# Performance work log

Hardware: AMD Instinct MI355X
Metric: run time of the kernel (lower is better)

Reference implementation:

```python
import jax, jax.numpy as jnp
import numpy as np
from jax import lax

WIN = 8
SHIFT = 4
NUM_HEADS = 8
DIM = 256
HIDDEN = 1024  # dim * mlp_ratio
EPS = 1e-5


def _layer_norm(x, g, b):
    mu = jnp.mean(x, axis=-1, keepdims=True)
    var = jnp.var(x, axis=-1, keepdims=True)
    return (x - mu) * lax.rsqrt(var + EPS) * g + b


def _window_partition(x, w):
    # x: [B,H,W,C] -> [B*nW, w*w, C]
    B, H, W, C = x.shape
    x = x.reshape(B, H // w, w, W // w, w, C)
    x = x.transpose(0, 1, 3, 2, 4, 5)
    return x.reshape(-1, w * w, C)


def _window_reverse(win, w, H, W):
    C = win.shape[-1]
    B = win.shape[0] // ((H // w) * (W // w))
    x = win.reshape(B, H // w, W // w, w, w, C)
    x = x.transpose(0, 1, 3, 2, 4, 5)
    return x.reshape(B, H, W, C)


def _rel_pos_index(w):
    coords = np.stack(np.meshgrid(np.arange(w), np.arange(w), indexing='ij'))
    cf = coords.reshape(2, -1)
    rel = cf[:, :, None] - cf[:, None, :]
    rel = rel.transpose(1, 2, 0).astype(np.int64)
    rel[:, :, 0] += w - 1
    rel[:, :, 1] += w - 1
    rel[:, :, 0] *= 2 * w - 1
    return rel.sum(-1)  # [w*w, w*w]


def _shift_mask(H, W, w, s):
    img = np.zeros((1, H, W, 1), dtype=np.float32)
    slices = (slice(0, -w), slice(-w, -s), slice(-s, None))
    cnt = 0
    for hs in slices:
        for ws in slices:
            img[:, hs, ws, :] = cnt
            cnt += 1
    mw = img.reshape(1, H // w, w, W // w, w, 1).transpose(0, 1, 3, 2, 4, 5).reshape(-1, w * w)
    diff = mw[:, None, :] - mw[:, :, None]
    return jnp.asarray(np.where(diff != 0, -100.0, 0.0).astype(np.float32))  # [nW,N,N]


def setup_inputs() -> dict:
    key = jax.random.key(0)
    ks = jax.random.split(key, 10)
    d, hid, h = DIM, HIDDEN, NUM_HEADS
    inp = {
        'x': jax.random.normal(ks[0], (2, 16384, d), dtype=jnp.float32),
        'norm1_g': jnp.ones((d,), jnp.float32),
        'norm1_b': jnp.zeros((d,), jnp.float32),
        'qkv_w': jax.random.normal(ks[1], (d, 3 * d), jnp.float32) * 0.02,
        'qkv_b': jnp.zeros((3 * d,), jnp.float32),
        'rel_bias_table': jax.random.normal(ks[2], ((2 * WIN - 1) ** 2, h), jnp.float32) * 0.02,
        'proj_w': jax.random.normal(ks[3], (d, d), jnp.float32) * 0.02,
        'proj_b': jnp.zeros((d,), jnp.float32),
        'norm2_g': jnp.ones((d,), jnp.float32),
        'norm2_b': jnp.zeros((d,), jnp.float32),
        'lin1_w': jax.random.normal(ks[4], (d, hid), jnp.float32) * 0.02,
        'lin1_b': jnp.zeros((hid,), jnp.float32),
        'dw_w': jax.random.normal(ks[5], (hid, 1, 3, 3), jnp.float32) * 0.1,
        'dw_b': jnp.zeros((hid,), jnp.float32),
        'lin2_w': jax.random.normal(ks[6], (hid, d), jnp.float32) * 0.02,
        'lin2_b': jnp.zeros((d,), jnp.float32),
    }
    return inp


def _forward(x, norm1_g, norm1_b, qkv_w, qkv_b, rel_bias_table, proj_w, proj_b,
             norm2_g, norm2_b, lin1_w, lin1_b, dw_w, dw_b, lin2_w, lin2_b):
    B, L, C = x.shape
    H = W = int(np.sqrt(L))
    h, dh = NUM_HEADS, C // NUM_HEADS
    N = WIN * WIN

    shortcut = x
    y = _layer_norm(x, norm1_g, norm1_b).reshape(B, H, W, C)
    if SHIFT > 0:
        y = jnp.roll(y, shift=(-SHIFT, -SHIFT), axis=(1, 2))
        attn_mask = _shift_mask(H, W, WIN, SHIFT)  # [nW,N,N]
    else:
        attn_mask = None

    xw = _window_partition(y, WIN)  # [B_, N, C]
    B_ = xw.shape[0]

    qkv = (xw @ qkv_w + qkv_b).reshape(B_, N, 3, h, dh).transpose(2, 0, 3, 1, 4)
    q, k, v = qkv[0], qkv[1], qkv[2]  # [B_, h, N, dh]
    q = q * (dh ** -0.5)
    attn = jnp.einsum('bhnd,bhmd->bhnm', q, k)

    rpi = _rel_pos_index(WIN)  # [N,N] numpy
    bias = rel_bias_table[rpi.reshape(-1)].reshape(N, N, h).transpose(2, 0, 1)
    attn = attn + bias[None]

    if attn_mask is not None:
        nW = attn_mask.shape[0]
        attn = attn.reshape(B_ // nW, nW, h, N, N) + attn_mask[None, :, None]
        attn = attn.reshape(B_, h, N, N)

    attn = jax.nn.softmax(attn, axis=-1)
    out = jnp.einsum('bhnm,bhmd->bhnd', attn, v).transpose(0, 2, 1, 3).reshape(B_, N, C)
    out = out @ proj_w + proj_b

    y = _window_reverse(out, WIN, H, W)
    if SHIFT > 0:
        y = jnp.roll(y, shift=(SHIFT, SHIFT), axis=(1, 2))
    x = shortcut + y.reshape(B, L, C)

    # LeFF
    z = _layer_norm(x, norm2_g, norm2_b)
    z = jax.nn.gelu(z @ lin1_w + lin1_b, approximate=False)
    z = z.reshape(B, H, W, HIDDEN).transpose(0, 3, 1, 2)  # NCHW
    z = lax.conv_general_dilated(z, dw_w, (1, 1), 'SAME',
                                 feature_group_count=HIDDEN,
                                 dimension_numbers=('NCHW', 'OIHW', 'NCHW'))
    z = jax.nn.gelu(z + dw_b[None, :, None, None], approximate=False)
    z = z.transpose(0, 2, 3, 1).reshape(B, L, HIDDEN)
    z = z @ lin2_w + lin2_b
    return x + z


def reference(x, norm1_g, norm1_b, qkv_w, qkv_b, rel_bias_table, proj_w, proj_b,
              norm2_g, norm2_b, lin1_w, lin1_b, dw_w, dw_b, lin2_w, lin2_b):
    return _forward(x, norm1_g, norm1_b, qkv_w, qkv_b, rel_bias_table, proj_w, proj_b,
                    norm2_g, norm2_b, lin1_w, lin1_b, dw_w, dw_b, lin2_w, lin2_b)
```

## Files before the change

### kernel.cpp

```cpp
#include <hip/hip_runtime.h>
#include <math.h>

#define BATCH 2
#define HW 128
#define CDIM 256
#define LTOK 16384
#define MTOK 32768
#define HEADS 8
#define DH 32
#define WINSZ 8
#define NWIN 64
#define HID 1024

typedef unsigned int  u32;
typedef unsigned short u16;

typedef __attribute__((ext_vector_type(8))) short bf16x8;
typedef __attribute__((ext_vector_type(4))) float f32x4;

__device__ __forceinline__ float gelu_f(float v) {
    return 0.5f * v * (1.f + erff(v * 0.70710678118654752f));
}

__device__ __forceinline__ u16 f2bf(float f) {
    u32 u = __float_as_uint(f);
    u32 r = (u + 0x7fffu + ((u >> 16) & 1u)) >> 16;
    return (u16)r;
}

__device__ __forceinline__ float4 ld4(const float* p) { return *(const float4*)p; }
__device__ __forceinline__ float4 ld4(const u16* p) {
    uint2 v = *(const uint2*)p;
    float4 r;
    r.x = __uint_as_float((v.x & 0xffffu) << 16);
    r.y = __uint_as_float(v.x & 0xffff0000u);
    r.z = __uint_as_float((v.y & 0xffffu) << 16);
    r.w = __uint_as_float(v.y & 0xffff0000u);
    return r;
}
__device__ __forceinline__ void st4(float* p, float4 v) { *(float4*)p = v; }
__device__ __forceinline__ void st4(u16* p, float4 v) {
    uint2 o;
    o.x = (u32)f2bf(v.x) | ((u32)f2bf(v.y) << 16);
    o.y = (u32)f2bf(v.z) | ((u32)f2bf(v.w) << 16);
    *(uint2*)p = o;
}
__device__ __forceinline__ float lds1(const float* p) { return *p; }
__device__ __forceinline__ float lds1(const u16* p) { return __uint_as_float(((u32)*p) << 16); }
__device__ __forceinline__ void sts1(float* p, float v) { *p = v; }
__device__ __forceinline__ void sts1(u16* p, float v) { *p = f2bf(v); }

__device__ __forceinline__ void ld8bf(const u16* p, float* v) {
    uint4 r = *(const uint4*)p;
    v[0] = __uint_as_float((r.x & 0xffffu) << 16);
    v[1] = __uint_as_float(r.x & 0xffff0000u);
    v[2] = __uint_as_float((r.y & 0xffffu) << 16);
    v[3] = __uint_as_float(r.y & 0xffff0000u);
    v[4] = __uint_as_float((r.z & 0xffffu) << 16);
    v[5] = __uint_as_float(r.z & 0xffff0000u);
    v[6] = __uint_as_float((r.w & 0xffffu) << 16);
    v[7] = __uint_as_float(r.w & 0xffff0000u);
}

__device__ __forceinline__ void glds16(const u16* g, u16* l) {
    __builtin_amdgcn_global_load_lds(
        (const __attribute__((address_space(1))) unsigned int*)g,
        (__attribute__((address_space(3))) unsigned int*)l, 16, 0, 0);
}

__global__ __launch_bounds__(256) void transpose_bf16_kernel(
    const float* __restrict__ in, u16* __restrict__ out, int K, int N)
{
    __shared__ float t[32][33];
    int bn = blockIdx.x * 32, bk = blockIdx.y * 32;
    int tx = threadIdx.x & 31, ty = threadIdx.x >> 5;
    #pragma unroll
    for (int i = 0; i < 32; i += 8)
        t[ty + i][tx] = in[(size_t)(bk + ty + i) * N + bn + tx];
    __syncthreads();
    #pragma unroll
    for (int i = 0; i < 32; i += 8)
        out[(size_t)(bn + ty + i) * K + bk + tx] = f2bf(t[tx][ty + i]);
}

__global__ __launch_bounds__(256) void dwprep_kernel(
    const float* __restrict__ in, float* __restrict__ out)
{
    int idx = blockIdx.x * 256 + threadIdx.x;
    if (idx < 9 * HID) {
        int ch = idx / 9, t = idx - ch * 9;
        out[t * HID + ch] = in[idx];
    }
}

template<typename TI, typename TO>
__global__ __launch_bounds__(256) void ln_kernel(
    const TI* __restrict__ x, const float* __restrict__ g,
    const float* __restrict__ b, TO* __restrict__ y)
{
    int wave = threadIdx.x >> 6;
    int lane = threadIdx.x & 63;
    int row = blockIdx.x * 4 + wave;
    const TI* xr = x + (size_t)row * CDIM;
    float4 v = ld4(&xr[lane * 4]);
    float s  = v.x + v.y + v.z + v.w;
    float s2 = v.x*v.x + v.y*v.y + v.z*v.z + v.w*v.w;
    #pragma unroll
    for (int off = 32; off > 0; off >>= 1) {
        s  += __shfl_xor(s,  off);
        s2 += __shfl_xor(s2, off);
    }
    float mu   = s * (1.f / CDIM);
    float var  = s2 * (1.f / CDIM) - mu * mu;
    float rstd = rsqrtf(var + 1e-5f);
    float4 gv = *(const float4*)&g[lane * 4];
    float4 bv = *(const float4*)&b[lane * 4];
    float4 o;
    o.x = (v.x - mu) * rstd * gv.x + bv.x;
    o.y = (v.y - mu) * rstd * gv.y + bv.y;
    o.z = (v.z - mu) * rstd * gv.z + bv.z;
    o.w = (v.w - mu) * rstd * gv.w + bv.w;
    st4(&y[(size_t)row * CDIM + lane * 4], o);
}

template<int EPI, int K, typename TR, typename TO>
__global__ __launch_bounds__(256) void mgemm_kernel(
    const u16* __restrict__ A, const u16* __restrict__ Bt,
    const float* __restrict__ bias, const TR* __restrict__ res,
    TO* __restrict__ Cc, int N, int gx)
{
    __shared__ u16 As[128 * 64];
    __shared__ u16 Bs[128 * 64];

    int tid  = threadIdx.x;
    int lane = tid & 63;
    int wave = tid >> 6;
    int l15  = lane & 15;
    int hi   = lane >> 4;
    int wr = wave >> 1, wc = wave & 1;

    int nwg = gridDim.x;
    int bid = blockIdx.x;
    int swz = (bid & 7) * (nwg >> 3) + (bid >> 3);
    int bx = swz % gx, by = swz / gx;
    size_t bm = (size_t)by * 128;
    size_t bn = (size_t)bx * 128;

    int srow8 = lane >> 3;
    int ce    = (lane & 7) * 8;

    int ar = wr * 64 + l15;
    int br = wc * 64 + l15;

    f32x4 acc[4][4] = {};

    for (int t = 0; t < K / 64; ++t) {
        int kt = t * 64;
        #pragma unroll
        for (int g = 0; g < 4; ++g) {
            int rowb = wave * 32 + g * 8;
            int row  = rowb + srow8;
            int col  = kt + (ce ^ ((row & 7) << 3));
            glds16(A  + (bm + row) * K + col, As + rowb * 64);
            glds16(Bt + (bn + row) * K + col, Bs + rowb * 64);
        }
        __syncthreads();

        #pragma unroll
        for (int ks = 0; ks < 2; ++ks) {
            int e = ks * 32 + hi * 8;
            bf16x8 af[4], bfv[4];
            #pragma unroll
            for (int m = 0; m < 4; ++m) {
                int row = ar + m * 16;
                af[m] = *(const bf16x8*)&As[row * 64 + (e ^ ((row & 7) << 3))];
            }
            #pragma unroll
            for (int n = 0; n < 4; ++n) {
                int row = br + n * 16;
                bfv[n] = *(const bf16x8*)&Bs[row * 64 + (e ^ ((row & 7) << 3))];
            }
            #pragma unroll
            for (int m = 0; m < 4; ++m)
                #pragma unroll
                for (int n = 0; n < 4; ++n)
                    acc[m][n] = __builtin_amdgcn_mfma_f32_16x16x32_bf16(
                        af[m], bfv[n], acc[m][n], 0, 0, 0);
        }
        __syncthreads();
    }

    int colb = (int)bn + wc * 64 + l15;
    int rowb = (int)bm + wr * 64 + hi * 4;
    #pragma unroll
    for (int n = 0; n < 4; ++n) {
        float bv = bias[colb + n * 16];
        #pragma unroll
        for (int m = 0; m < 4; ++m) {
            #pragma unroll
            for (int r = 0; r < 4; ++r) {
                int row = rowb + m * 16 + r;
                float v = acc[m][n][r] + bv;
                if (EPI == 1) v += lds1(&res[(size_t)row * N + colb + n * 16]);
                if (EPI == 2) v = gelu_f(v);
                sts1(&Cc[(size_t)row * N + colb + n * 16], v);
            }
        }
    }
}

__global__ __launch_bounds__(512) void fused_qkv_attn_kernel(
    const u16* __restrict__ yn, const u16* __restrict__ qkv_wt,
    const float* __restrict__ qkv_b, const float* __restrict__ bias_table,
    u16* __restrict__ out)
{
    __shared__ u16 lds[8][4096];

    int tid  = threadIdx.x;
    int lane = tid & 63;
    int head = tid >> 6;
    int l15  = lane & 15;
    int hi   = lane >> 4;
    int w  = blockIdx.x;
    int b  = w >> 8;
    int ww = w & 255;
    int wr = ww >> 4, wc = ww & 15;
    u16* L = lds[head];

    auto tokof = [&](int n) -> int {
        int si = (wr * WINSZ + (n >> 3) + 4) & 127;
        int sj = (wc * WINSZ + (n & 7) + 4) & 127;
        return b * LTOK + si * HW + sj;
    };
    auto labelof = [&](int n) -> int {
        int i = wr * WINSZ + (n >> 3);
        int j = wc * WINSZ + (n & 7);
        int li = (i < 120) ? 0 : (i < 124 ? 1 : 2);
        int lj = (j < 120) ? 0 : (j < 124 ? 1 : 2);
        return li * 3 + lj;
    };

    const u16* arow[4];
    #pragma unroll
    for (int m = 0; m < 4; ++m)
        arow[m] = yn + (size_t)tokof(m * 16 + l15) * CDIM + hi * 8;

    f32x4 qa[4][2] = {}, ka[4][2] = {};
    #pragma unroll
    for (int kb = 0; kb < 8; ++kb) {
        bf16x8 a[4];
        #pragma unroll
        for (int m = 0; m < 4; ++m)
            a[m] = *(const bf16x8*)(arow[m] + kb * 32);
        #pragma unroll
        for (int nf = 0; nf < 2; ++nf) {
            const u16* wp = qkv_wt +
                (size_t)(head * 32 + nf * 16 + l15) * CDIM + kb * 32 + hi * 8;
            bf16x8 bq = *(const bf16x8*)wp;
            bf16x8 bk = *(const bf16x8*)(wp + 256 * CDIM);
            #pragma unroll
            for (int m = 0; m < 4; ++m) {
                qa[m][nf] = __builtin_amdgcn_mfma_f32_16x16x32_bf16(a[m], bq, qa[m][nf], 0, 0, 0);
                ka[m][nf] = __builtin_amdgcn_mfma_f32_16x16x32_bf16(a[m], bk, ka[m][nf], 0, 0, 0);
            }
        }
    }
    #pragma unroll
    for (int nf = 0; nf < 2; ++nf) {
        int d = nf * 16 + l15;
        float bq = qkv_b[head * 32 + d];
        float bk = qkv_b[256 + head * 32 + d];
        int g = nf * 2 + (l15 >> 3);
        #pragma unroll
        for (int m = 0; m < 4; ++m)
            #pragma unroll
            for (int r = 0; r < 4; ++r) {
                int tok = m * 16 + hi * 4 + r;
                int ad = tok * 32 + ((g ^ r ^ hi) << 3) + (d & 7);
                L[ad]        = f2bf(qa[m][nf][r] + bq);
                L[2048 + ad] = f2bf(ka[m][nf][r] + bk);
            }
    }
    bf16x8 qf[4], kf[4];
    {
        int sz = (hi ^ (l15 & 3) ^ ((l15 >> 2) & 3)) << 3;
        #pragma unroll
        for (int m = 0; m < 4; ++m) {
            int ra = (m * 16 + l15) * 32 + sz;
            qf[m] = *(const bf16x8*)&L[ra];
            kf[m] = *(const bf16x8*)&L[2048 + ra];
        }
    }

    f32x4 va[4][2] = {};
    #pragma unroll
    for (int kb = 0; kb < 8; ++kb) {
        bf16x8 a[4];
        #pragma unroll
        for (int m = 0; m < 4; ++m)
            a[m] = *(const bf16x8*)(arow[m] + kb * 32);
        #pragma unroll
        for (int nf = 0; nf < 2; ++nf) {
            const u16* wp = qkv_wt +
                (size_t)(512 + head * 32 + nf * 16 + l15) * CDIM + kb * 32 + hi * 8;
            bf16x8 bv = *(const bf16x8*)wp;
            #pragma unroll
            for (int m = 0; m < 4; ++m)
                va[m][nf] = __builtin_amdgcn_mfma_f32_16x16x32_bf16(a[m], bv, va[m][nf], 0, 0, 0);
        }
    }
    #pragma unroll
    for (int nf = 0; nf < 2; ++nf) {
        int d = nf * 16 + l15;
        float bv = qkv_b[512 + head * 32 + d];
        #pragma unroll
        for (int m = 0; m < 4; ++m)
            #pragma unroll
            for (int r = 0; r < 4; ++r) {
                int tok = m * 16 + hi * 4 + r;
                int av = d * 64 + (((tok >> 3) ^ (d & 7)) << 3) + (tok & 7);
                L[av] = f2bf(va[m][nf][r] + bv);
            }
    }
    bf16x8 vf[2][2];
    #pragma unroll
    for (int nf = 0; nf < 2; ++nf) {
        int d = nf * 16 + l15;
        #pragma unroll
        for (int ks = 0; ks < 2; ++ks) {
            int rv = d * 64 + (((ks * 4 + hi) ^ (d & 7)) << 3);
            vf[nf][ks] = *(const bf16x8*)&L[rv];
        }
    }

    f32x4 s[4][4];
    #pragma unroll
    for (int m = 0; m < 4; ++m)
        #pragma unroll
        for (int n = 0; n < 4; ++n) {
            f32x4 z = {0.f, 0.f, 0.f, 0.f};
            s[m][n] = __builtin_amdgcn_mfma_f32_16x16x32_bf16(qf[m], kf[n], z, 0, 0, 0);
        }

    int klbl[4];
    #pragma unroll
    for (int n = 0; n < 4; ++n) klbl[n] = labelof(n * 16 + l15);

    const float SCALE = 0.17677669529663687f;
    float inv[4][4];
    #pragma unroll
    for (int m = 0; m < 4; ++m) {
        #pragma unroll
        for (int r = 0; r < 4; ++r) {
            int q = m * 16 + hi * 4 + r;
            int qlbl = labelof(q);
            int rq = q >> 3, cq = q & 7;
            float v[4];
            #pragma unroll
            for (int n = 0; n < 4; ++n) {
                int kn = n * 16 + l15;
                int idx = (rq - (kn >> 3) + 7) * 15 + (cq - (kn & 7) + 7);
                float bv = bias_table[idx * HEADS + head];
                v[n] = s[m][n][r] * SCALE + bv + ((klbl[n] != qlbl) ? -100.f : 0.f);
            }
            float rmax = fmaxf(fmaxf(v[0], v[1]), fmaxf(v[2], v[3]));
            #pragma unroll
            for (int off = 1; off < 16; off <<= 1)
                rmax = fmaxf(rmax, __shfl_xor(rmax, off));
            float p0 = __expf(v[0] - rmax), p1 = __expf(v[1] - rmax);
            float p2 = __expf(v[2] - rmax), p3 = __expf(v[3] - rmax);
            float ls = p0 + p1 + p2 + p3;
            #pragma unroll
            for (int off = 1; off < 16; off <<= 1)
                ls += __shfl_xor(ls, off);
            inv[m][r] = 1.f / ls;
            int sw = (q & 7) << 3;
            L[q * 64 + ((0 * 16 + l15) ^ sw)] = f2bf(p0);
            L[q * 64 + ((1 * 16 + l15) ^ sw)] = f2bf(p1);
            L[q * 64 + ((2 * 16 + l15) ^ sw)] = f2bf(p2);
            L[q * 64 + ((3 * 16 + l15) ^ sw)] = f2bf(p3);
        }
    }

    f32x4 o[4][2] = {};
    #pragma unroll
    for (int ks = 0; ks < 2; ++ks) {
        #pragma unroll
        for (int m = 0; m < 4; ++m) {
            int row = m * 16 + l15;
            int colb = (ks * 32 + hi * 8) ^ ((row & 7) << 3);
            bf16x8 pa = *(const bf16x8*)&L[row * 64 + colb];
            #pragma unroll
            for (int nf = 0; nf < 2; ++nf)
                o[m][nf] = __builtin_amdgcn_mfma_f32_16x16x32_bf16(
                    pa, vf[nf][ks], o[m][nf], 0, 0, 0);
        }
    }

    #pragma unroll
    for (int m = 0; m < 4; ++m) {
        #pragma unroll
        for (int r = 0; r < 4; ++r) {
            int q = m * 16 + hi * 4 + r;
            int t = tokof(q);
            u16* op = out + (size_t)t * CDIM + head * DH + l15;
            float iv = inv[m][r];
            op[0]  = f2bf(o[m][0][r] * iv);
            op[16] = f2bf(o[m][1][r] * iv);
        }
    }
}

__global__ __launch_bounds__(256) void dwconv_kernel(
    const u16* __restrict__ h, const float* __restrict__ wt9,
    const float* __restrict__ bias, u16* __restrict__ out)
{
    int blk = blockIdx.x;
    int b   = blk >> 11;
    int rem = blk & 2047;
    int i   = rem >> 4;
    int jt  = rem & 15;
    int cg  = (threadIdx.x & 127) * 8;
    int j0  = jt * 8 + (threadIdx.x >> 7) * 4;

    float acc[4][8] = {};
    const u16* base = h + (size_t)b * LTOK * HID + cg;

    #pragma unroll
    for (int di = 0; di < 3; ++di) {
        int ii = i + di - 1;
        if (ii < 0 || ii >= HW) continue;
        const u16* rowp = base + (size_t)ii * HW * HID;
        float v[6][8];
        #pragma unroll
        for (int cc = 0; cc < 6; ++cc) {
            int jj = j0 - 1 + cc;
            if (jj >= 0 && jj < HW) {
                ld8bf(&rowp[(size_t)jj * HID], v[cc]);
            } else {
                #pragma unroll
                for (int q = 0; q < 8; ++q) v[cc][q] = 0.f;
            }
        }
        #pragma unroll
        for (int t = 0; t < 3; ++t) {
            const float* wp = &wt9[(di * 3 + t) * HID + cg];
            float4 wa = *(const float4*)wp;
            float4 wb = *(const float4*)(wp + 4);
            float w[8] = {wa.x, wa.y, wa.z, wa.w, wb.x, wb.y, wb.z, wb.w};
            #pragma unroll
            for (int p = 0; p < 4; ++p)
                #pragma unroll
                for (int q = 0; q < 8; ++q)
                    acc[p][q] += v[p + t][q] * w[q];
        }
    }

    float4 ba = *(const float4*)&bias[cg];
    float4 bb = *(const float4*)&bias[cg + 4];
    float bs[8] = {ba.x, ba.y, ba.z, ba.w, bb.x, bb.y, bb.z, bb.w};
    u16* ob = out + ((size_t)b * LTOK + (size_t)i * HW + j0) * HID + cg;
    #pragma unroll
    for (int p = 0; p < 4; ++p) {
        u32 o[4];
        #pragma unroll
        for (int q = 0; q < 4; ++q) {
            u16 lo = f2bf(gelu_f(acc[p][2 * q] + bs[2 * q]));
            u16 hi = f2bf(gelu_f(acc[p][2 * q + 1] + bs[2 * q + 1]));
            o[q] = (u32)lo | ((u32)hi << 16);
        }
        *(uint4*)(ob + (size_t)p * HID) = make_uint4(o[0], o[1], o[2], o[3]);
    }
}

extern "C" void kernel_launch(void* const* d_in, const int* in_sizes, int n_in,
                              void* d_out, int out_size, void* d_ws, size_t ws_size,
                              hipStream_t stream) {
    const float* x      = (const float*)d_in[0];
    const float* n1g    = (const float*)d_in[1];
    const float* n1b    = (const float*)d_in[2];
    const float* qkv_w  = (const float*)d_in[3];
    const float* qkv_b  = (const float*)d_in[4];
    const float* relb   = (const float*)d_in[5];
    const float* proj_w = (const float*)d_in[6];
    const float* proj_b = (const float*)d_in[7];
    const float* n2g    = (const float*)d_in[8];
    const float* n2b    = (const float*)d_in[9];
    const float* lin1_w = (const float*)d_in[10];
    const float* lin1_b = (const float*)d_in[11];
    const float* dw_w   = (const float*)d_in[12];
    const float* dw_b   = (const float*)d_in[13];
    const float* lin2_w = (const float*)d_in[14];
    const float* lin2_b = (const float*)d_in[15];
    float* out = (float*)d_out;

    u16* ws16 = (u16*)d_ws;
    const size_t M8 = (size_t)MTOK * CDIM;
    u16* yn      = ws16;
    u16* attn    = ws16 + M8;
    u16* x1      = ws16 + 4 * M8;
    u16* yn2     = ws16;
    u16* hbuf    = ws16 + 5 * M8;
    u16* h2      = ws16;
    u16* qkv_wt  = ws16 + 5 * M8;
    u16* proj_wt = qkv_wt + 768 * 256;
    u16* lin1_wt = ws16 + 2 * M8;
    u16* lin2_wt = ws16 + 5 * M8;
    float* wt9   = (float*)d_out;

    transpose_bf16_kernel<<<dim3(768 / 32, 256 / 32), 256, 0, stream>>>(qkv_w, qkv_wt, 256, 768);
    transpose_bf16_kernel<<<dim3(256 / 32, 256 / 32), 256, 0, stream>>>(proj_w, proj_wt, 256, 256);
    ln_kernel<float, u16><<<MTOK / 4, 256, 0, stream>>>(x, n1g, n1b, yn);
    fused_qkv_attn_kernel<<<512, 512, 0, stream>>>(yn, qkv_wt, qkv_b, relb, attn);
    transpose_bf16_kernel<<<dim3(1024 / 32, 256 / 32), 256, 0, stream>>>(lin1_w, lin1_wt, 256, 1024);
    dwprep_kernel<<<36, 256, 0, stream>>>(dw_w, wt9);
    mgemm_kernel<1, CDIM, float, u16><<<(CDIM / 128) * (MTOK / 128), 256, 0, stream>>>(
        attn, proj_wt, proj_b, x, x1, CDIM, CDIM / 128);
    ln_kernel<u16, u16><<<MTOK / 4, 256, 0, stream>>>(x1, n2g, n2b, yn2);
    mgemm_kernel<2, CDIM, float, u16><<<(HID / 128) * (MTOK / 128), 256, 0, stream>>>(
        yn2, lin1_wt, lin1_b, (const float*)nullptr, hbuf, HID, HID / 128);
    dwconv_kernel<<<BATCH * 2048, 256, 0, stream>>>(hbuf, wt9, dw_b, h2);
    transpose_bf16_kernel<<<dim3(256 / 32, 1024 / 32), 256, 0, stream>>>(lin2_w, lin2_wt, 1024, 256);
    mgemm_kernel<1, HID, u16, float><<<(CDIM / 128) * (MTOK / 128), 256, 0, stream>>>(
        h2, lin2_wt, lin2_b, x1, out, CDIM, CDIM / 128);

    (void)in_sizes; (void)n_in; (void)out_size; (void)ws_size;
}
```

Before: 276.8 us.

## Fuse projection GEMM, residual add and second LayerNorm into one kernel

Replaces the proj GEMM plus separate LayerNorm kernel with a single kernel where each 64-row block computes the full 256-wide output. It adds bias and the residual, reduces per-row statistics across waves through LDS, and writes both x1 and the normalized yn2. This removes one launch and the round trip of re-reading x1 for the norm. The dwconv block index is also swizzled across groups of 8 to change the block-to-CU mapping. The variance is computed with a single-pass E[x²]-mu² formula, and x1 is now rounded to bf16 after normalization rather than before.

After: 297.0 us. 1.07x slower.

```diff
diff --git a/kernel.cpp b/kernel.cpp
--- a/kernel.cpp
+++ b/kernel.cpp
@@ -209,6 +209,126 @@
     }
 }
 
+__global__ __launch_bounds__(256) void proj_ln_kernel(
+    const u16* __restrict__ A, const u16* __restrict__ Bt,
+    const float* __restrict__ bias, const float* __restrict__ x,
+    const float* __restrict__ g2, const float* __restrict__ b2,
+    u16* __restrict__ x1, u16* __restrict__ yn2)
+{
+    __shared__ u16 As[64 * 64];
+    __shared__ u16 Bs[256 * 64];
+    float* stats = (float*)As;
+
+    int tid  = threadIdx.x;
+    int lane = tid & 63;
+    int wave = tid >> 6;
+    int l15  = lane & 15;
+    int hi   = lane >> 4;
+
+    int nwg = gridDim.x;
+    int bid = blockIdx.x;
+    int swz = (bid & 7) * (nwg >> 3) + (bid >> 3);
+    size_t bm = (size_t)swz * 64;
+
+    int srow8 = lane >> 3;
+    int ce    = (lane & 7) * 8;
+
+    f32x4 acc[4][4] = {};
+
+    for (int t = 0; t < 4; ++t) {
+        int kt = t * 64;
+        #pragma unroll
+        for (int g = 0; g < 2; ++g) {
+            int rowb = wave * 16 + g * 8;
+            int row  = rowb + srow8;
+            int col  = kt + (ce ^ ((row & 7) << 3));
+            glds16(A + (bm + row) * CDIM + col, As + rowb * 64);
+        }
+        #pragma unroll
+        for (int g = 0; g < 8; ++g) {
+            int rowb = wave * 64 + g * 8;
+            int row  = rowb + srow8;
+            int col  = kt + (ce ^ ((row & 7) << 3));
+            glds16(Bt + (size_t)row * CDIM + col, Bs + rowb * 64);
+        }
+        __syncthreads();
+
+        #pragma unroll
+        for (int ks = 0; ks < 2; ++ks) {
+            int e = ks * 32 + hi * 8;
+            bf16x8 af[4], bfv[4];
+            #pragma unroll
+            for (int m = 0; m < 4; ++m) {
+                int row = m * 16 + l15;
+                af[m] = *(const bf16x8*)&As[row * 64 + (e ^ ((row & 7) << 3))];
+            }
+            #pragma unroll
+            for (int n = 0; n < 4; ++n) {
+                int row = wave * 64 + n * 16 + l15;
+                bfv[n] = *(const bf16x8*)&Bs[row * 64 + (e ^ ((row & 7) << 3))];
+            }
+            #pragma unroll
+            for (int m = 0; m < 4; ++m)
+                #pragma unroll
+                for (int n = 0; n < 4; ++n)
+                    acc[m][n] = __builtin_amdgcn_mfma_f32_16x16x32_bf16(
+                        af[m], bfv[n], acc[m][n], 0, 0, 0);
+        }
+        __syncthreads();
+    }
+
+    int colb = wave * 64 + l15;
+    #pragma unroll
+    for (int m = 0; m < 4; ++m) {
+        #pragma unroll
+        for (int r = 0; r < 4; ++r) {
+            int row_l = m * 16 + hi * 4 + r;
+            size_t grow = bm + row_l;
+            float s1 = 0.f, s2 = 0.f;
+            #pragma unroll
+            for (int n = 0; n < 4; ++n) {
+                int col = colb + n * 16;
+                float v = acc[m][n][r] + bias[col] + x[grow * CDIM + col];
+                acc[m][n][r] = v;
+                s1 += v; s2 += v * v;
+            }
+            #pragma unroll
+            for (int off = 1; off < 16; off <<= 1) {
+                s1 += __shfl_xor(s1, off);
+                s2 += __shfl_xor(s2, off);
+            }
+            if (l15 == 0) {
+                stats[row_l * 8 + wave * 2 + 0] = s1;
+                stats[row_l * 8 + wave * 2 + 1] = s2;
+            }
+        }
+    }
+    __syncthreads();
+
+    #pragma unroll
+    for (int m = 0; m < 4; ++m) {
+        #pragma unroll
+        for (int r = 0; r < 4; ++r) {
+            int row_l = m * 16 + hi * 4 + r;
+            size_t grow = bm + row_l;
+            float s1 = stats[row_l * 8 + 0] + stats[row_l * 8 + 2] +
+                       stats[row_l * 8 + 4] + stats[row_l * 8 + 6];
+            float s2 = stats[row_l * 8 + 1] + stats[row_l * 8 + 3] +
+                       stats[row_l * 8 + 5] + stats[row_l * 8 + 7];
+            float mu   = s1 * (1.f / CDIM);
+            float var  = s2 * (1.f / CDIM) - mu * mu;
+            float rstd = rsqrtf(var + 1e-5f);
+            #pragma unroll
+            for (int n = 0; n < 4; ++n) {
+                int col = colb + n * 16;
+                float v = acc[m][n][r];
+                x1[grow * CDIM + col]  = f2bf(v);
+                yn2[grow * CDIM + col] = f2bf((v - mu) * rstd * g2[col] + b2[col]);
+            }
+        }
+    }
+}
+
 __global__ __launch_bounds__(512) void fused_qkv_attn_kernel(
     const u16* __restrict__ yn, const u16* __restrict__ qkv_wt,
     const float* __restrict__ qkv_b, const float* __restrict__ bias_table,
@@ -415,7 +535,8 @@
     const u16* __restrict__ h, const float* __restrict__ wt9,
     const float* __restrict__ bias, u16* __restrict__ out)
 {
-    int blk = blockIdx.x;
+    int bid = blockIdx.x;
+    int blk = (bid & 7) * ((int)gridDim.x >> 3) + (bid >> 3);
     int b   = blk >> 11;
     int rem = blk & 2047;
     int i   = rem >> 4;
@@ -514,9 +635,8 @@
     fused_qkv_attn_kernel<<<512, 512, 0, stream>>>(yn, qkv_wt, qkv_b, relb, attn);
     transpose_bf16_kernel<<<dim3(1024 / 32, 256 / 32), 256, 0, stream>>>(lin1_w, lin1_wt, 256, 1024);
     dwprep_kernel<<<36, 256, 0, stream>>>(dw_w, wt9);
-    mgemm_kernel<1, CDIM, float, u16><<<(CDIM / 128) * (MTOK / 128), 256, 0, stream>>>(
-        attn, proj_wt, proj_b, x, x1, CDIM, CDIM / 128);
-    ln_kernel<u16, u16><<<MTOK / 4, 256, 0, stream>>>(x1, n2g, n2b, yn2);
+    proj_ln_kernel<<<MTOK / 64, 256, 0, stream>>>(
+        attn, proj_wt, proj_b, x, n2g, n2b, x1, yn2);
     mgemm_kernel<2, CDIM, float, u16><<<(HID / 128) * (MTOK / 128), 256, 0, stream>>>(
         yn2, lin1_wt, lin1_b, (const float*)nullptr, hbuf, HID, HID / 128);
     dwconv_kernel<<<BATCH * 2048, 256, 0, stream>>>(hbuf, wt9, dw_b, h2);
```
